# Kernel optimization log

Hardware: AMD Instinct MI355X
Metric: run time of the kernel (lower is better)

## Reference

```python
import jax, jax.numpy as jnp
import numpy as np

N = 100000
E = 1600000
D_IN, D_HID, D_OUT = 128, 128, 128


def gcn_conv(x, edge_index, W, b):
    """PyG GCNConv with default symmetric normalization and added self-loops.
    out = D^{-1/2} (A + I) D^{-1/2} (x W) + b, edge weights = 1.
    """
    n = x.shape[0]
    h = x @ W                                   # [N, D_out]
    src, dst = edge_index[0], edge_index[1]     # messages flow src -> dst
    ones = jnp.ones(src.shape[0], dtype=x.dtype)
    # degree includes the self-loop (+1), computed on the target index as in PyG
    deg = jax.ops.segment_sum(ones, dst, num_segments=n) + 1.0  # [N]
    dinv = jax.lax.rsqrt(deg)                   # deg >= 1 so safe
    norm = dinv[src] * dinv[dst]                # [E]
    msg = h[src] * norm[:, None]                # [E, D_out]
    agg = jax.ops.segment_sum(msg, dst, num_segments=n)
    # self-loop contribution: norm = dinv_i * dinv_i = 1/deg_i
    out = agg + h * (dinv * dinv)[:, None] + b
    return out


def layer_norm(x, gamma, beta, eps=1e-5):
    mu = jnp.mean(x, axis=-1, keepdims=True)
    var = jnp.mean(jnp.square(x - mu), axis=-1, keepdims=True)
    return (x - mu) * jax.lax.rsqrt(var + eps) * gamma + beta


def setup_inputs() -> dict:
    key = jax.random.key(0)
    ks = jax.random.split(key, 8)
    x = jax.random.normal(ks[0], (N, D_IN), dtype=jnp.float32)
    edge_index = jax.random.randint(ks[1], (2, E), 0, N, dtype=jnp.int64)
    s1 = 1.0 / np.sqrt(D_IN)
    s2 = 1.0 / np.sqrt(D_HID)
    W1 = jax.random.uniform(ks[2], (D_IN, D_HID), jnp.float32, -s1, s1)
    b1 = jnp.zeros((D_HID,), jnp.float32)
    W2 = jax.random.uniform(ks[3], (D_HID, D_OUT), jnp.float32, -s2, s2)
    b2 = jnp.zeros((D_OUT,), jnp.float32)
    gamma = jnp.ones((D_OUT,), jnp.float32)
    beta = jnp.zeros((D_OUT,), jnp.float32)
    return {"x": x, "edge_index": edge_index, "W1": W1, "b1": b1,
            "W2": W2, "b2": b2, "gamma": gamma, "beta": beta}


def reference(x, edge_index, W1, b1, W2, b2, gamma, beta):
    h = gcn_conv(x, edge_index, W1, b1)
    h = jax.nn.relu(h)
    # dropout is identity in eval mode (deterministic reference)
    h = gcn_conv(h, edge_index, W2, b2)
    return layer_norm(h, gamma, beta)
```

## Files before the change

### kernel.cpp

```cpp
#include <hip/hip_runtime.h>


#define N_NODES 100000
#define N_EDGES 1600000
#define NBLK_N  391
#define NB      196
#define BKT_CAP 8960
#define BIN_GRID 391
#define GEMM_GRID 1563

typedef unsigned int  u32;
typedef unsigned short u16;
typedef unsigned char u8;
typedef unsigned long long u64;
typedef __attribute__((ext_vector_type(8))) short bf16x8;
typedef __attribute__((ext_vector_type(4))) float f32x4;

__device__ __forceinline__ float bflo(u32 u){ return __uint_as_float(u << 16); }
__device__ __forceinline__ float bfhi(u32 u){ return __uint_as_float(u & 0xFFFF0000u); }
__device__ __forceinline__ u32 f2b(float f){
  u32 u = __float_as_uint(f);
  return (u + 0x7FFFu + ((u >> 16) & 1u)) >> 16;
}
__device__ __forceinline__ u32 pack2(float a, float b){ return f2b(a) | (f2b(b) << 16); }
__device__ __forceinline__ u32 clampN(int s){
  u32 u = (u32)s;
  return (u < (u32)N_NODES) ? u : (u32)(N_NODES - 1);
}

__global__ __launch_bounds__(64) void detect(const int* __restrict__ ei,
                                             int* __restrict__ flags){
  int l = threadIdx.x;
  int nzodd = (ei[2 * l + 1] != 0) ? 1 : 0;
  #pragma unroll
  for (int o = 32; o > 0; o >>= 1) nzodd += __shfl_xor(nzodd, o, 64);
  if (l == 0) flags[1] = (nzodd == 0) ? 1 : 0;
}


__global__ __launch_bounds__(256) void prep_frags(const float* __restrict__ W1,
                                                  const float* __restrict__ W2,
                                                  u16* __restrict__ w1f,
                                                  u16* __restrict__ w2f,
                                                  u32* __restrict__ bucket_fill){
  const float* W = blockIdx.x ? W2 : W1;
  u16* dst = blockIdx.x ? w2f : w1f;
  const int tid = threadIdx.x;
  #pragma unroll
  for (int i = 0; i < 8; ++i){
    int fid   = tid + i * 256;
    int lane  = fid & 63;
    int kb    = (fid >> 6) & 3;
    int ntile = fid >> 8;
    int n  = ntile * 16 + (lane & 15);
    int k0 = kb * 32 + (lane >> 4) * 8;
    u16 tmp[8];
    #pragma unroll
    for (int j = 0; j < 8; ++j) tmp[j] = (u16)f2b(W[(k0 + j) * 128 + n]);
    *(bf16x8*)(dst + (size_t)fid * 8) = *(const bf16x8*)tmp;
  }
  if (blockIdx.x == 0 && tid < NB) bucket_fill[tid] = 0;
}


__device__ __forceinline__ void gemm_tail(const u16* __restrict__ wfrag,
                                          const bf16x8 afrag[4],
                                          int rowbase, int lane,
                                          u16* __restrict__ Hout, int nrows){
  const int m = lane & 15, q = lane >> 4;
  f32x4 acc[8];
  #pragma unroll
  for (int n = 0; n < 8; ++n) acc[n] = (f32x4){0.f, 0.f, 0.f, 0.f};
  #pragma unroll
  for (int n = 0; n < 8; ++n){
    #pragma unroll
    for (int kb = 0; kb < 4; ++kb){
      bf16x8 bfrag = *(const bf16x8*)(wfrag + ((size_t)(n * 4 + kb) * 64 + lane) * 8);
      acc[n] = __builtin_amdgcn_mfma_f32_16x16x32_bf16(afrag[kb], bfrag, acc[n], 0, 0, 0);
    }
  }
  #pragma unroll
  for (int r = 0; r < 4; ++r){
    int orow = rowbase + q * 4 + r;
    if (orow < nrows){
      u16* Or = Hout + (size_t)orow * 128 + m;
      #pragma unroll
      for (int n = 0; n < 8; ++n) Or[n * 16] = (u16)f2b(acc[n][r]);
    }
  }
}

__device__ __forceinline__ void gemm_f32_body(const u16* __restrict__ wfragG,
                                              const float* __restrict__ A,
                                              u16* __restrict__ Hout, int nrows, int bid){
  const int lane = threadIdx.x & 63;
  const int wv   = threadIdx.x >> 6;
  const int rowbase = bid * 64 + wv * 16;
  const int row  = rowbase + (lane & 15);
  const int rowc = (row < nrows) ? row : (nrows - 1);
  const int q    = lane >> 4;
  bf16x8 afrag[4];
  const float* Ar = A + (size_t)rowc * 128;
  #pragma unroll
  for (int kb = 0; kb < 4; ++kb){
    f32x4 p0 = *(const f32x4*)(Ar + kb * 32 + q * 8);
    f32x4 p1 = *(const f32x4*)(Ar + kb * 32 + q * 8 + 4);
    bf16x8 f;
    f[0] = (short)f2b(p0[0]); f[1] = (short)f2b(p0[1]);
    f[2] = (short)f2b(p0[2]); f[3] = (short)f2b(p0[3]);
    f[4] = (short)f2b(p1[0]); f[5] = (short)f2b(p1[1]);
    f[6] = (short)f2b(p1[2]); f[7] = (short)f2b(p1[3]);
    afrag[kb] = f;
  }
  gemm_tail(wfragG, afrag, rowbase, lane, Hout, nrows);
}

__device__ __forceinline__ void gemm_bf16_body(const u16* __restrict__ wfragG,
                                               const u16* __restrict__ A,
                                               u16* __restrict__ Hout, int nrows, int bid){
  const int lane = threadIdx.x & 63;
  const int wv   = threadIdx.x >> 6;
  const int rowbase = bid * 64 + wv * 16;
  const int row  = rowbase + (lane & 15);
  const int rowc = (row < nrows) ? row : (nrows - 1);
  const int q    = lane >> 4;
  bf16x8 afrag[4];
  const u16* Ar = A + (size_t)rowc * 128;
  #pragma unroll
  for (int kb = 0; kb < 4; ++kb)
    afrag[kb] = *(const bf16x8*)(Ar + kb * 32 + q * 8);
  gemm_tail(wfragG, afrag, rowbase, lane, Hout, nrows);
}


__device__ __forceinline__ void binA_body(u32* cnt ,
                                          const int* __restrict__ ei,
                                          u32* __restrict__ binned,
                                          u32* __restrict__ bucket_fill, int bb){
  u32* gbase = cnt + 256;
  u32* flagp = cnt + 512;
  const int tid = threadIdx.x;
  cnt[tid] = 0;
  if (tid < 64){
    int nz = (ei[2 * tid + 1] != 0) ? 1 : 0;
    u64 b = __ballot(nz);
    if (tid == 0) *flagp = (b == 0ull) ? 1u : 0u;
  }
  __syncthreads();
  const int i64  = (int)*flagp;
  const int base = bb * 4096;
  u32 pk[16], rk[16], bk[16];
  #pragma unroll
  for (int j = 0; j < 16; ++j){
    int e = base + tid + j * 256;
    bk[j] = 0xFFFFFFFFu;
    if (e < N_EDGES){
      int dsti = i64 ? ei[2 * N_EDGES + 2 * e] : ei[N_EDGES + e];
      int srci = i64 ? ei[2 * e]               : ei[e];
      u32 ud = clampN(dsti), us = clampN(srci);
      u32 b = ud >> 9;
      bk[j] = b;
      pk[j] = us | ((ud & 511u) << 17);
      rk[j] = atomicAdd(&cnt[b], 1u);
    }
  }
  __syncthreads();
  u32 c = cnt[tid];
  u32 old = 0;
  if (c) old = atomicAdd(&bucket_fill[tid < NB ? tid : 0], tid < NB ? c : 0u);
  gbase[tid] = old;
  __syncthreads();
  #pragma unroll
  for (int j = 0; j < 16; ++j){
    if (bk[j] != 0xFFFFFFFFu){
      u32 idx = gbase[bk[j]] + rk[j];
      if (idx < BKT_CAP) binned[(size_t)bk[j] * BKT_CAP + idx] = pk[j];
    }
  }
}


__global__ __launch_bounds__(256) void fused_gemm_bin(const float* __restrict__ A,
                                                      const u16* __restrict__ w1frag,
                                                      u16* __restrict__ Hout,
                                                      const int* __restrict__ ei,
                                                      u32* __restrict__ binned,
                                                      u32* __restrict__ bucket_fill){
  __shared__ u32 binsmem[520];
  if (blockIdx.x < GEMM_GRID){
    gemm_f32_body(w1frag, A, Hout, N_NODES, blockIdx.x);
  } else {
    binA_body(binsmem, ei, binned, bucket_fill, blockIdx.x - GEMM_GRID);
  }
}

__global__ __launch_bounds__(256) void gemm_f32in(const float* __restrict__ A,
                                                  const u16* __restrict__ wfragG,
                                                  u16* __restrict__ Hout){
  gemm_f32_body(wfragG, A, Hout, N_NODES, blockIdx.x);
}
__global__ __launch_bounds__(256) void gemm_bf16in(const u16* __restrict__ A,
                                                   const u16* __restrict__ wfragG,
                                                   u16* __restrict__ Hout){
  gemm_bf16_body(wfragG, A, Hout, N_NODES, blockIdx.x);
}


__global__ __launch_bounds__(256) void fill_sort(const u32* __restrict__ binned,
                                                 const u32* __restrict__ bucket_fill,
                                                 int* __restrict__ offs,
                                                 float* __restrict__ dinv,
                                                 int* __restrict__ srclist){
  __shared__ u32 cnt[512];
  __shared__ u32 sc[512];
  __shared__ u32 red[256];
  const int b   = blockIdx.x;
  const int tid = threadIdx.x;
  cnt[tid] = 0; cnt[tid + 256] = 0;
  __syncthreads();

  u32 n = bucket_fill[b]; if (n > BKT_CAP) n = BKT_CAP;
  const u32* eb = binned + (size_t)b * BKT_CAP;

  for (u32 i = tid; i < n; i += 256)
    atomicAdd(&cnt[eb[i] >> 17], 1u);

  u32 v = 0;
  if (tid < b && tid < NB){
    u32 f = bucket_fill[tid];
    v = (f > BKT_CAP) ? BKT_CAP : f;
  }
  red[tid] = v;
  __syncthreads();
  for (int o = 128; o > 0; o >>= 1){
    if (tid < o) red[tid] += red[tid + o];
    __syncthreads();
  }
  const u32 base = red[0];
  __syncthreads();

  u32 pair = cnt[2 * tid] + cnt[2 * tid + 1];
  red[tid] = pair;
  __syncthreads();
  for (int o = 1; o < 256; o <<= 1){
    u32 add = (tid >= o) ? red[tid - o] : 0;
    __syncthreads();
    red[tid] += add;
    __syncthreads();
  }
  u32 pex = red[tid] - pair;
  sc[2 * tid]     = pex;
  sc[2 * tid + 1] = pex + cnt[2 * tid];
  __syncthreads();

  const u32 basenode = (u32)b << 9;
  #pragma unroll
  for (int h = 0; h < 2; ++h){
    u32 l = tid + h * 256;
    u32 node = basenode + l;
    if (node < (u32)N_NODES){
      offs[node] = (int)(base + sc[l]);
      dinv[node] = rsqrtf((float)cnt[l] + 1.0f);
    }
  }
  if (b == NB - 1 && tid == 0) offs[N_NODES] = (int)(base + n);

  __syncthreads();
  cnt[tid] = 0; cnt[tid + 256] = 0;
  __syncthreads();
  for (u32 i = tid; i < n; i += 256){
    u32 pk = eb[i];
    u32 d  = pk >> 17;
    u32 r  = atomicAdd(&cnt[d], 1u);
    srclist[base + sc[d] + r] = (int)(pk & 0x1FFFFu);
  }
}


__global__ __launch_bounds__(256) void count_deg(const int* __restrict__ ei,
                                                 const int* __restrict__ flags,
                                                 int* __restrict__ deg){
  int e   = blockIdx.x * 256 + threadIdx.x;
  int i64 = flags[1];
  int dst = i64 ? ei[2 * N_EDGES + 2 * e] : ei[N_EDGES + e];
  if ((unsigned)dst < (unsigned)N_NODES) atomicAdd(&deg[dst], 1);
}

__global__ __launch_bounds__(256) void fill_edges(const int* __restrict__ ei,
                                                  const int* __restrict__ flags,
                                                  int* __restrict__ woff,
                                                  int* __restrict__ srclist){
  int e   = blockIdx.x * 256 + threadIdx.x;
  int i64 = flags[1];
  int dst = i64 ? ei[2 * N_EDGES + 2 * e] : ei[N_EDGES + e];
  int src = i64 ? ei[2 * e]               : ei[e];
  if ((unsigned)dst < (unsigned)N_NODES){
    int p = atomicAdd(&woff[dst], 1);
    if ((unsigned)p < (unsigned)N_EDGES) srclist[p] = clampN(src);
  }
}

__global__ __launch_bounds__(256) void scan1(const int* __restrict__ deg,
                                             int* __restrict__ offs,
                                             int* __restrict__ bsum,
                                             float* __restrict__ dinv){
  __shared__ int sh[256];
  int t = threadIdx.x;
  int i = blockIdx.x * 256 + t;
  int v = (i < N_NODES) ? deg[i] : 0;
  if (i < N_NODES) dinv[i] = rsqrtf((float)v + 1.0f);
  sh[t] = v;
  __syncthreads();
  for (int o = 1; o < 256; o <<= 1){
    int add = (t >= o) ? sh[t - o] : 0;
    __syncthreads();
    sh[t] += add;
    __syncthreads();
  }
  if (i < N_NODES) offs[i] = sh[t] - v;
  if (t == 255)    bsum[blockIdx.x] = sh[255];
}

__global__ __launch_bounds__(512) void scan2(const int* __restrict__ bsum,
                                             int* __restrict__ bofs){
  __shared__ int sh[512];
  int t = threadIdx.x;
  int v = (t < NBLK_N) ? bsum[t] : 0;
  sh[t] = v;
  __syncthreads();
  for (int o = 1; o < 512; o <<= 1){
    int add = (t >= o) ? sh[t - o] : 0;
    __syncthreads();
    sh[t] += add;
    __syncthreads();
  }
  if (t < NBLK_N) bofs[t] = sh[t] - v;
}

__global__ __launch_bounds__(256) void finalize_offs(int* __restrict__ offs,
                                                     const int* __restrict__ bofs,
                                                     int* __restrict__ woff){
  int i = blockIdx.x * 256 + threadIdx.x;
  if (i < N_NODES){
    int o = offs[i] + bofs[blockIdx.x];
    offs[i] = o;
    woff[i] = o;
  }
  if (i == 0) offs[N_NODES] = N_EDGES;
}


#define GATHER_EDGE(sv, A0, A1)                         \
  { u32 s_ = (u32)(sv);                                 \
    float w_ = dinv[s_];                                \
    u32 h_ = H[s_ * 64 + lane];                         \
    A0 = fmaf(w_, bflo(h_), A0);                        \
    A1 = fmaf(w_, bfhi(h_), A1); }

#define GATHER_BODY                                     \
  int beg = offs[node], end = offs[node + 1];           \
  if (end > N_EDGES) end = N_EDGES;                     \
  if (beg < 0 || beg > end) beg = end;                  \
  float a0 = 0.f, a1 = 0.f, c0 = 0.f, c1 = 0.f;         \
  int e = beg;                                          \
  for (; e + 8 <= end; e += 8){                         \
    int s0=srcl[e],s1=srcl[e+1],s2=srcl[e+2],s3=srcl[e+3]; \
    int s4=srcl[e+4],s5=srcl[e+5],s6=srcl[e+6],s7=srcl[e+7]; \
    GATHER_EDGE(s0,a0,a1) GATHER_EDGE(s1,c0,c1)         \
    GATHER_EDGE(s2,a0,a1) GATHER_EDGE(s3,c0,c1)         \
    GATHER_EDGE(s4,a0,a1) GATHER_EDGE(s5,c0,c1)         \
    GATHER_EDGE(s6,a0,a1) GATHER_EDGE(s7,c0,c1)         \
  }                                                     \
  for (; e + 4 <= end; e += 4){                         \
    int s0=srcl[e],s1=srcl[e+1],s2=srcl[e+2],s3=srcl[e+3]; \
    GATHER_EDGE(s0,a0,a1) GATHER_EDGE(s1,c0,c1)         \
    GATHER_EDGE(s2,a0,a1) GATHER_EDGE(s3,c0,c1)         \
  }                                                     \
  for (; e < end; ++e){ int s0=srcl[e]; GATHER_EDGE(s0,a0,a1) } \
  a0 += c0;  a1 += c1;                                  \
  float di = dinv[node];                                \
  u32 hs = H[(u32)node * 64 + lane];                    \
  float v0 = fmaf(a0, di, fmaf(bflo(hs), di * di, bb0)); \
  float v1 = fmaf(a1, di, fmaf(bfhi(hs), di * di, bb1));

__global__ __launch_bounds__(256) void gather_relu(const int* __restrict__ offs,
                                                   const int* __restrict__ srcl,
                                                   const u32* __restrict__ H,
                                                   const float* __restrict__ dinv,
                                                   const float* __restrict__ bias,
                                                   u32* __restrict__ X2){
  const int node = blockIdx.x * 4 + (threadIdx.x >> 6);
  const int lane = threadIdx.x & 63;
  const float bb0 = bias[2 * lane], bb1 = bias[2 * lane + 1];
  GATHER_BODY
  X2[(u32)node * 64 + lane] = pack2(fmaxf(v0, 0.f), fmaxf(v1, 0.f));
}

__global__ __launch_bounds__(256) void gather_ln(const int* __restrict__ offs,
                                                 const int* __restrict__ srcl,
                                                 const u32* __restrict__ H,
                                                 const float* __restrict__ dinv,
                                                 const float* __restrict__ bias,
                                                 const float* __restrict__ gamma,
                                                 const float* __restrict__ beta,
                                                 float* __restrict__ out){
  const int node = blockIdx.x * 4 + (threadIdx.x >> 6);
  const int lane = threadIdx.x & 63;
  const float bb0 = bias[2 * lane], bb1 = bias[2 * lane + 1];
  GATHER_BODY

  float s2 = v0 + v1;
  #pragma unroll
  for (int o = 32; o > 0; o >>= 1) s2 += __shfl_xor(s2, o, 64);
  float mu = s2 * 0.0078125f;
  float d0 = v0 - mu, d1 = v1 - mu;
  float qq = d0 * d0 + d1 * d1;
  #pragma unroll
  for (int o = 32; o > 0; o >>= 1) qq += __shfl_xor(qq, o, 64);
  float rr = rsqrtf(qq * 0.0078125f + 1e-5f);

  float g0 = gamma[2 * lane], g1 = gamma[2 * lane + 1];
  float t0 = beta[2 * lane],  t1 = beta[2 * lane + 1];
  *(float2*)(out + (size_t)node * 128 + 2 * lane) =
      make_float2(fmaf(d0 * rr, g0, t0), fmaf(d1 * rr, g1, t1));
}


extern "C" void kernel_launch(void* const* d_in, const int* in_sizes, int n_in,
                              void* d_out, int out_size, void* d_ws, size_t ws_size,
                              hipStream_t stream){
  const float* x  = (const float*)d_in[0];
  const int*   ei = (const int*)d_in[1];
  const float* W1 = (const float*)d_in[2];
  const float* b1 = (const float*)d_in[3];
  const float* W2 = (const float*)d_in[4];
  const float* b2 = (const float*)d_in[5];
  const float* gm = (const float*)d_in[6];
  const float* bt = (const float*)d_in[7];

  char* ws = (char*)d_ws;
  size_t off = 0;
  auto carve = [&](size_t bytes) -> void* {
    void* p = ws + off;
    off = (off + bytes + 255) & ~(size_t)255;
    return p;
  };
  int*   flags       = (int*)  carve(64);
  u16*   w1frag      = (u16*)  carve(128 * 128 * 2);
  u16*   w2frag      = (u16*)  carve(128 * 128 * 2);
  u32*   bucket_fill = (u32*)  carve(NB * 4);
  int*   offs        = (int*)  carve((size_t)(N_NODES + 1) * 4);
  float* dinv        = (float*)carve((size_t)N_NODES * 4);
  int*   srclist     = (int*)  carve((size_t)N_EDGES * 4);
  int*   deg         = (int*)  carve((size_t)N_NODES * 4);
  int*   bsum        = (int*)  carve(2048);
  int*   bofs        = (int*)  carve(2048);

  size_t bin_bytes = (size_t)NB * BKT_CAP * 4;
  u32* binned = (u32*)carve(bin_bytes);
  bool use_binned = (ws_size >= off);
  if (!use_binned) off = (size_t)((char*)binned - ws);

  size_t h_bytes = (size_t)N_NODES * 128 * 2;
  u32* H1 = (u32*)d_out;
  u32* X2 = (u32*)d_out + 6400000;
  u32* H2 = (ws_size >= off + h_bytes) ? (u32*)carve(h_bytes) : (u32*)d_in[0];

  prep_frags <<<2, 256, 0, stream>>>(W1, W2, w1frag, w2frag, bucket_fill);

  if (use_binned){
    fused_gemm_bin<<<GEMM_GRID + BIN_GRID, 256, 0, stream>>>(x, w1frag, (u16*)H1, ei,
                                                             binned, bucket_fill);
    fill_sort     <<<NB, 256, 0, stream>>>(binned, bucket_fill, offs, dinv, srclist);
  } else {
    hipMemsetAsync(deg, 0, (size_t)N_NODES * 4, stream);
    detect        <<<1,             64,  0, stream>>>(ei, flags);
    count_deg     <<<N_EDGES / 256, 256, 0, stream>>>(ei, flags, deg);
    scan1         <<<NBLK_N,        256, 0, stream>>>(deg, offs, bsum, dinv);
    scan2         <<<1,             512, 0, stream>>>(bsum, bofs);
    finalize_offs <<<NBLK_N,        256, 0, stream>>>(offs, bofs, deg );
    fill_edges    <<<N_EDGES / 256, 256, 0, stream>>>(ei, flags, deg , srclist);
    gemm_f32in    <<<GEMM_GRID,     256, 0, stream>>>(x, w1frag, (u16*)H1);
  }

  gather_relu <<<N_NODES / 4, 256, 0, stream>>>(offs, srclist, H1, dinv, b1, X2);
  gemm_bf16in <<<GEMM_GRID,   256, 0, stream>>>((const u16*)X2, w2frag, (u16*)H2);
  gather_ln   <<<N_NODES / 4, 256, 0, stream>>>(offs, srclist, H2, dinv, b2, gm, bt,
                                                (float*)d_out);
}
```

Measured before the change: 312.3 us.

## Overlap layer-1 GEMM with fill_sort and fuse weight prep into binning

Restructures the CSR build pipeline. Weight fragment prep now runs inside the binning kernel, and the layer-1 GEMM moves from the binning launch into the fill_sort launch. Buckets shrink from 512 to 256 destination nodes, so there are 391 buckets with smaller capacity, and the prefix scan in fill_sort becomes one entry per thread. The aim is to drop a launch and hide the fill_sort tail behind GEMM work, at the cost of an extra memset and more global bucket atomics.

Measured after the change: 307.5 us. About the same (-1.5%).

```diff
diff --git a/kernel.cpp b/kernel.cpp
--- a/kernel.cpp
+++ b/kernel.cpp
@@ -4,8 +4,8 @@
 #define N_NODES 100000
 #define N_EDGES 1600000
 #define NBLK_N  391
-#define NB      196
-#define BKT_CAP 8960
+#define NB      391
+#define BKT_CAP 4736
 #define BIN_GRID 391
 #define GEMM_GRID 1563
 
@@ -38,14 +38,8 @@
 }
 
 
-__global__ __launch_bounds__(256) void prep_frags(const float* __restrict__ W1,
-                                                  const float* __restrict__ W2,
-                                                  u16* __restrict__ w1f,
-                                                  u16* __restrict__ w2f,
-                                                  u32* __restrict__ bucket_fill){
-  const float* W = blockIdx.x ? W2 : W1;
-  u16* dst = blockIdx.x ? w2f : w1f;
-  const int tid = threadIdx.x;
+__device__ __forceinline__ void prep_body(const float* __restrict__ W,
+                                          u16* __restrict__ dst, int tid){
   #pragma unroll
   for (int i = 0; i < 8; ++i){
     int fid   = tid + i * 256;
@@ -59,7 +53,13 @@
     for (int j = 0; j < 8; ++j) tmp[j] = (u16)f2b(W[(k0 + j) * 128 + n]);
     *(bf16x8*)(dst + (size_t)fid * 8) = *(const bf16x8*)tmp;
   }
-  if (blockIdx.x == 0 && tid < NB) bucket_fill[tid] = 0;
+}
+
+__global__ __launch_bounds__(256) void prep_frags(const float* __restrict__ W1,
+                                                  const float* __restrict__ W2,
+                                                  u16* __restrict__ w1f,
+                                                  u16* __restrict__ w2f){
+  prep_body(blockIdx.x ? W2 : W1, blockIdx.x ? w2f : w1f, threadIdx.x);
 }
 
 
@@ -133,14 +133,15 @@
 }
 
 
-__device__ __forceinline__ void binA_body(u32* cnt ,
+__device__ __forceinline__ void binA_body(u32* smem ,
                                           const int* __restrict__ ei,
                                           u32* __restrict__ binned,
                                           u32* __restrict__ bucket_fill, int bb){
-  u32* gbase = cnt + 256;
-  u32* flagp = cnt + 512;
+  u32* cnt   = smem;
+  u32* gbase = smem + NB;
+  u32* flagp = smem + 2 * NB;
   const int tid = threadIdx.x;
-  cnt[tid] = 0;
+  for (int i = tid; i < NB; i += 256) cnt[i] = 0;
   if (tid < 64){
     int nz = (ei[2 * tid + 1] != 0) ? 1 : 0;
     u64 b = __ballot(nz);
@@ -158,17 +159,17 @@
       int dsti = i64 ? ei[2 * N_EDGES + 2 * e] : ei[N_EDGES + e];
       int srci = i64 ? ei[2 * e]               : ei[e];
       u32 ud = clampN(dsti), us = clampN(srci);
-      u32 b = ud >> 9;
+      u32 b = ud >> 8;
       bk[j] = b;
-      pk[j] = us | ((ud & 511u) << 17);
+      pk[j] = us | ((ud & 255u) << 17);
       rk[j] = atomicAdd(&cnt[b], 1u);
     }
   }
   __syncthreads();
-  u32 c = cnt[tid];
-  u32 old = 0;
-  if (c) old = atomicAdd(&bucket_fill[tid < NB ? tid : 0], tid < NB ? c : 0u);
-  gbase[tid] = old;
+  for (int i = tid; i < NB; i += 256){
+    u32 c = cnt[i];
+    gbase[i] = c ? atomicAdd(&bucket_fill[i], c) : 0u;
+  }
   __syncthreads();
   #pragma unroll
   for (int j = 0; j < 16; ++j){
@@ -180,100 +181,112 @@
 }
 
 
-__global__ __launch_bounds__(256) void fused_gemm_bin(const float* __restrict__ A,
-                                                      const u16* __restrict__ w1frag,
-                                                      u16* __restrict__ Hout,
-                                                      const int* __restrict__ ei,
-                                                      u32* __restrict__ binned,
-                                                      u32* __restrict__ bucket_fill){
-  __shared__ u32 binsmem[520];
-  if (blockIdx.x < GEMM_GRID){
-    gemm_f32_body(w1frag, A, Hout, N_NODES, blockIdx.x);
+__global__ __launch_bounds__(256) void bin_prep(const int* __restrict__ ei,
+                                                u32* __restrict__ binned,
+                                                u32* __restrict__ bucket_fill,
+                                                const float* __restrict__ W1,
+                                                const float* __restrict__ W2,
+                                                u16* __restrict__ w1f,
+                                                u16* __restrict__ w2f){
+  __shared__ u32 smem[2 * NB + 1];
+  if (blockIdx.x < BIN_GRID){
+    binA_body(smem, ei, binned, bucket_fill, blockIdx.x);
   } else {
-    binA_body(binsmem, ei, binned, bucket_fill, blockIdx.x - GEMM_GRID);
-  }
-}
-
-__global__ __launch_bounds__(256) void gemm_f32in(const float* __restrict__ A,
-                                                  const u16* __restrict__ wfragG,
-                                                  u16* __restrict__ Hout){
-  gemm_f32_body(wfragG, A, Hout, N_NODES, blockIdx.x);
-}
-__global__ __launch_bounds__(256) void gemm_bf16in(const u16* __restrict__ A,
-                                                   const u16* __restrict__ wfragG,
-                                                   u16* __restrict__ Hout){
-  gemm_bf16_body(wfragG, A, Hout, N_NODES, blockIdx.x);
-}
-
-
-__global__ __launch_bounds__(256) void fill_sort(const u32* __restrict__ binned,
-                                                 const u32* __restrict__ bucket_fill,
-                                                 int* __restrict__ offs,
-                                                 float* __restrict__ dinv,
-                                                 int* __restrict__ srclist){
-  __shared__ u32 cnt[512];
-  __shared__ u32 sc[512];
-  __shared__ u32 red[256];
-  const int b   = blockIdx.x;
+    int pb = blockIdx.x - BIN_GRID;
+    prep_body(pb ? W2 : W1, pb ? w2f : w1f, threadIdx.x);
+  }
+}
+
+
+__device__ __forceinline__ void fill_sort_body(u32* smem ,
+                                               const u32* __restrict__ binned,
+                                               const u32* __restrict__ bucket_fill,
+                                               int* __restrict__ offs,
+                                               float* __restrict__ dinv,
+                                               int* __restrict__ srclist, int b){
+  u32* cnt = smem;
+  u32* sc  = smem + 256;
+  u32* red = smem + 512;
   const int tid = threadIdx.x;
-  cnt[tid] = 0; cnt[tid + 256] = 0;
-  __syncthreads();
+  cnt[tid] = 0;
+
+  u32 v = 0;
+  for (int i = tid; i < b; i += 256){
+    u32 f = bucket_fill[i];
+    v += (f > BKT_CAP) ? BKT_CAP : f;
+  }
+  red[tid] = v;
+  __syncthreads();
+  for (int o = 128; o > 0; o >>= 1){
+    if (tid < o) red[tid] += red[tid + o];
+    __syncthreads();
+  }
+  const u32 base = red[0];
 
   u32 n = bucket_fill[b]; if (n > BKT_CAP) n = BKT_CAP;
   const u32* eb = binned + (size_t)b * BKT_CAP;
 
   for (u32 i = tid; i < n; i += 256)
     atomicAdd(&cnt[eb[i] >> 17], 1u);
-
-  u32 v = 0;
-  if (tid < b && tid < NB){
-    u32 f = bucket_fill[tid];
-    v = (f > BKT_CAP) ? BKT_CAP : f;
-  }
-  red[tid] = v;
-  __syncthreads();
-  for (int o = 128; o > 0; o >>= 1){
-    if (tid < o) red[tid] += red[tid + o];
-    __syncthreads();
-  }
-  const u32 base = red[0];
-  __syncthreads();
-
-  u32 pair = cnt[2 * tid] + cnt[2 * tid + 1];
-  red[tid] = pair;
+  __syncthreads();
+
+  u32 own = cnt[tid];
+  sc[tid] = own;
   __syncthreads();
   for (int o = 1; o < 256; o <<= 1){
-    u32 add = (tid >= o) ? red[tid - o] : 0;
-    __syncthreads();
-    red[tid] += add;
-    __syncthreads();
-  }
-  u32 pex = red[tid] - pair;
-  sc[2 * tid]     = pex;
-  sc[2 * tid + 1] = pex + cnt[2 * tid];
-  __syncthreads();
-
-  const u32 basenode = (u32)b << 9;
-  #pragma unroll
-  for (int h = 0; h < 2; ++h){
-    u32 l = tid + h * 256;
-    u32 node = basenode + l;
-    if (node < (u32)N_NODES){
-      offs[node] = (int)(base + sc[l]);
-      dinv[node] = rsqrtf((float)cnt[l] + 1.0f);
-    }
+    u32 add = (tid >= o) ? sc[tid - o] : 0;
+    __syncthreads();
+    sc[tid] += add;
+    __syncthreads();
+  }
+  u32 pex = sc[tid] - own;
+
+  const u32 node = ((u32)b << 8) + tid;
+  if (node < (u32)N_NODES){
+    offs[node] = (int)(base + pex);
+    dinv[node] = rsqrtf((float)own + 1.0f);
   }
   if (b == NB - 1 && tid == 0) offs[N_NODES] = (int)(base + n);
 
   __syncthreads();
-  cnt[tid] = 0; cnt[tid + 256] = 0;
-  __syncthreads();
+  sc[tid]  = pex;
+  cnt[tid] = 0;
+  __syncthreads();
+
   for (u32 i = tid; i < n; i += 256){
     u32 pk = eb[i];
     u32 d  = pk >> 17;
     u32 r  = atomicAdd(&cnt[d], 1u);
     srclist[base + sc[d] + r] = (int)(pk & 0x1FFFFu);
   }
+}
+
+
+__global__ __launch_bounds__(256) void fused_fs_gemm(const u32* __restrict__ binned,
+                                                     const u32* __restrict__ bucket_fill,
+                                                     int* __restrict__ offs,
+                                                     float* __restrict__ dinv,
+                                                     int* __restrict__ srclist,
+                                                     const float* __restrict__ A,
+                                                     const u16* __restrict__ w1frag,
+                                                     u16* __restrict__ Hout){
+  __shared__ u32 smem[768];
+  if (blockIdx.x < NB){
+    fill_sort_body(smem, binned, bucket_fill, offs, dinv, srclist, blockIdx.x);
+  } else {
+    gemm_f32_body(w1frag, A, Hout, N_NODES, blockIdx.x - NB);
+  }
+}
+
+__global__ __launch_bounds__(256) void gemm_f32in(const float* __restrict__ A,
+                                                  const u16* __restrict__ wfragG,
+                                                  u16* __restrict__ Hout){
+  gemm_f32_body(wfragG, A, Hout, N_NODES, blockIdx.x);
+}
+__global__ __launch_bounds__(256) void gemm_bf16in(const u16* __restrict__ A,
+                                                   const u16* __restrict__ wfragG,
+                                                   u16* __restrict__ Hout){
+  gemm_bf16_body(wfragG, A, Hout, N_NODES, blockIdx.x);
 }
 
 
@@ -466,13 +479,14 @@
   u32* X2 = (u32*)d_out + 6400000;
   u32* H2 = (ws_size >= off + h_bytes) ? (u32*)carve(h_bytes) : (u32*)d_in[0];
 
-  prep_frags <<<2, 256, 0, stream>>>(W1, W2, w1frag, w2frag, bucket_fill);
-
   if (use_binned){
-    fused_gemm_bin<<<GEMM_GRID + BIN_GRID, 256, 0, stream>>>(x, w1frag, (u16*)H1, ei,
-                                                             binned, bucket_fill);
-    fill_sort     <<<NB, 256, 0, stream>>>(binned, bucket_fill, offs, dinv, srclist);
+    hipMemsetAsync(bucket_fill, 0, NB * 4, stream);
+    bin_prep      <<<BIN_GRID + 2, 256, 0, stream>>>(ei, binned, bucket_fill,
+                                                     W1, W2, w1frag, w2frag);
+    fused_fs_gemm <<<NB + GEMM_GRID, 256, 0, stream>>>(binned, bucket_fill, offs, dinv,
+                                                       srclist, x, w1frag, (u16*)H1);
   } else {
+    prep_frags    <<<2,             256, 0, stream>>>(W1, W2, w1frag, w2frag);
     hipMemsetAsync(deg, 0, (size_t)N_NODES * 4, stream);
     detect        <<<1,             64,  0, stream>>>(ei, flags);
     count_deg     <<<N_EDGES / 256, 256, 0, stream>>>(ei, flags, deg);
```
